# Performance work log

Measured on AMD Instinct MI355X. Metric: run time of the kernel, lower is better.

The kernel has to match this reference:

```python
import jax, jax.numpy as jnp
import numpy as np

B, IN, OUT = 8192, 1024, 1024
GRID_SIZE, SPLINE_ORDER = 5, 3
GRID_LO, GRID_HI = -1.0, 1.0
LN_EPS = 1e-5


def make_grid():
    h = (GRID_HI - GRID_LO) / GRID_SIZE
    g = jnp.linspace(GRID_LO - h * SPLINE_ORDER, GRID_HI + h * SPLINE_ORDER,
                     GRID_SIZE + 2 * SPLINE_ORDER + 1, dtype=jnp.float32)
    return jnp.broadcast_to(g, (IN, g.shape[0]))  # [IN, 12]


def setup_inputs() -> dict:
    key = jax.random.key(0)
    k1, k2, k3 = jax.random.split(key, 3)
    # kaiming_uniform_ linear: bound = sqrt(3/fan_in)
    bw_bound = float(np.sqrt(3.0 / IN))
    sw_bound = float(np.sqrt(3.0 / (IN * 8)))
    return {
        "x": jax.random.normal(k1, (B, IN), dtype=jnp.float32),
        "base_weight": jax.random.uniform(k2, (OUT, IN), minval=-bw_bound, maxval=bw_bound, dtype=jnp.float32),
        "spline_weight": jax.random.uniform(k3, (OUT, IN, GRID_SIZE + SPLINE_ORDER), minval=-sw_bound, maxval=sw_bound, dtype=jnp.float32),
        "grid": make_grid(),
        "ln_gamma": jnp.ones((OUT,), dtype=jnp.float32),
        "ln_beta": jnp.zeros((OUT,), dtype=jnp.float32),
        "prelu_a": jnp.full((1,), 0.25, dtype=jnp.float32),
    }


def _bspline_bases(x, grid):
    # x: [B, IN]; grid: [IN, 12] -> bases: [B, IN, GRID_SIZE+SPLINE_ORDER]
    xu = x[:, :, None]                      # [B, IN, 1]
    g = grid[None, :, :]                    # [1, IN, 12]
    bases = ((xu >= g[..., :-1]) & (xu < g[..., 1:])).astype(x.dtype)
    for k in range(1, SPLINE_ORDER + 1):
        left = g[..., :-(k + 1)]
        right = g[..., k:-1]
        g_rshift = g[..., k + 1:]
        g_lshift = g[..., 1:-k]
        dr = right - left
        dd = g_rshift - g_lshift
        dr = jnp.where(dr == 0, jnp.ones_like(dr), dr)
        dd = jnp.where(dd == 0, jnp.ones_like(dd), dd)
        bases = (xu - left) / dr * bases[..., :-1] + (g_rshift - xu) / dd * bases[..., 1:]
    return bases


def reference(x, base_weight, spline_weight, grid, ln_gamma, ln_beta, prelu_a):
    base_out = jnp.dot(jax.nn.gelu(x, approximate=False), base_weight.T)  # [B, OUT]
    bases = _bspline_bases(x, grid)                                        # [B, IN, 8]
    spline_out = jnp.einsum('bik,oik->bo', bases, spline_weight)           # [B, OUT]
    y = base_out + spline_out
    mu = jnp.mean(y, axis=-1, keepdims=True)
    var = jnp.mean(jnp.square(y - mu), axis=-1, keepdims=True)
    yn = (y - mu) * jax.lax.rsqrt(var + LN_EPS) * ln_gamma + ln_beta
    return jnp.where(yn >= 0, yn, prelu_a * yn)
```

## Files before the change

### kernel.cpp

```cpp
#include <hip/hip_runtime.h>
#include <hip/hip_bf16.h>

typedef __attribute__((ext_vector_type(8))) short bf16x8;
typedef __attribute__((ext_vector_type(4))) float f32x4;

#define KTOT 9216
#define KHALF 4608
#define NB   8192
#define NIN  1024
#define NOUT 1024

__device__ __forceinline__ void load_lds16(const void* g, void* l) {
  __builtin_amdgcn_global_load_lds(
      (const __attribute__((address_space(1))) void*)g,
      (__attribute__((address_space(3))) void*)l, 16, 0, 0);
}

__global__ void prep(const float* __restrict__ x,
                     const float* __restrict__ grid,
                     __hip_bfloat16* __restrict__ A,
                     const float* __restrict__ bw,
                     const float* __restrict__ sw,
                     __hip_bfloat16* __restrict__ W) {
  if (blockIdx.x < 4096) {
    const int tid = blockIdx.x * blockDim.x + threadIdx.x;
    const int i  = tid & (NIN - 1);
    const int b0 = (tid >> 10) << 3;

    float g[12];
#pragma unroll
    for (int j = 0; j < 12; ++j) g[j] = grid[j];

    float invdr1[10], invdd1[10], invdr2[9], invdd2[9], invdr3[8], invdd3[8];
#pragma unroll
    for (int j = 0; j < 10; ++j) {
      invdr1[j] = __builtin_amdgcn_rcpf(g[j + 1] - g[j]);
      invdd1[j] = __builtin_amdgcn_rcpf(g[j + 2] - g[j + 1]);
    }
#pragma unroll
    for (int j = 0; j < 9; ++j) {
      invdr2[j] = __builtin_amdgcn_rcpf(g[j + 2] - g[j]);
      invdd2[j] = __builtin_amdgcn_rcpf(g[j + 3] - g[j + 1]);
    }
#pragma unroll
    for (int j = 0; j < 8; ++j) {
      invdr3[j] = __builtin_amdgcn_rcpf(g[j + 3] - g[j]);
      invdd3[j] = __builtin_amdgcn_rcpf(g[j + 4] - g[j + 1]);
    }

    for (int bb = 0; bb < 8; ++bb) {
      const int b = b0 + bb;
      const float xv = x[(size_t)b * NIN + i];
      const float ge = 0.5f * xv * (1.0f + erff(xv * 0.70710678118654752f));
      __hip_bfloat16* Arow = A + (size_t)b * KTOT;
      Arow[i] = __float2bfloat16(ge);

      float bas[11];
#pragma unroll
      for (int j = 0; j < 11; ++j)
        bas[j] = (xv >= g[j] && xv < g[j + 1]) ? 1.0f : 0.0f;
#pragma unroll
      for (int j = 0; j < 10; ++j)
        bas[j] = (xv - g[j]) * invdr1[j] * bas[j] + (g[j + 2] - xv) * invdd1[j] * bas[j + 1];
#pragma unroll
      for (int j = 0; j < 9; ++j)
        bas[j] = (xv - g[j]) * invdr2[j] * bas[j] + (g[j + 3] - xv) * invdd2[j] * bas[j + 1];
#pragma unroll
      for (int j = 0; j < 8; ++j)
        bas[j] = (xv - g[j]) * invdr3[j] * bas[j] + (g[j + 4] - xv) * invdd3[j] * bas[j + 1];

      union { __hip_bfloat16 h[8]; uint4 v; } u;
#pragma unroll
      for (int k = 0; k < 8; ++k) u.h[k] = __float2bfloat16(bas[k]);
      *reinterpret_cast<uint4*>(Arow + NIN + i * 8) = u.v;
    }
  } else {
    const int idx = (blockIdx.x - 4096) * blockDim.x + threadIdx.x;
    const int o  = idx / 1152;
    const int c8 = (idx - o * 1152) * 8;
    const float* src = (c8 < 1024) ? (bw + (size_t)o * 1024 + c8)
                                   : (sw + (size_t)o * 8192 + (c8 - 1024));
    float4 f0 = reinterpret_cast<const float4*>(src)[0];
    float4 f1 = reinterpret_cast<const float4*>(src)[1];
    union { __hip_bfloat16 h[8]; uint4 v; } u;
    u.h[0] = __float2bfloat16(f0.x); u.h[1] = __float2bfloat16(f0.y);
    u.h[2] = __float2bfloat16(f0.z); u.h[3] = __float2bfloat16(f0.w);
    u.h[4] = __float2bfloat16(f1.x); u.h[5] = __float2bfloat16(f1.y);
    u.h[6] = __float2bfloat16(f1.z); u.h[7] = __float2bfloat16(f1.w);
    *reinterpret_cast<uint4*>(W + (size_t)o * KTOT + c8) = u.v;
  }
}

__global__ __launch_bounds__(512, 2)
void gemm_8ph(const __hip_bfloat16* __restrict__ A,
              const __hip_bfloat16* __restrict__ Bw,
              float* __restrict__ P0,
              float* __restrict__ P1w) {
  __shared__ char smem[131072];

  const int tid  = threadIdx.x;
  const int lane = tid & 63;
  const int wave = tid >> 6;
  const int wr = wave >> 2;
  const int wc = wave & 3;

  const int orig = blockIdx.x;
  const int bid  = (orig & 7) * 32 + (orig >> 3);
  const int ks    = bid & 1;
  const int tileN = (bid >> 1) & 3;
  const int tileM = bid >> 3;
  const size_t brow = (size_t)tileM * 256;
  const size_t bcol = (size_t)tileN * 256;
  const int kbeg = ks * KHALF;

  const __hip_bfloat16* Ab = A  + brow * KTOT;
  const __hip_bfloat16* Bb = Bw + bcol * KTOT;
  float* C = ks ? P1w : P0;

  const int swsrc = ((tid & 7) ^ ((tid >> 3) & 7)) * 8;
  const __hip_bfloat16* srcA = Ab + (size_t)(tid >> 3) * KTOT + kbeg + swsrc;
  const __hip_bfloat16* srcB = Bb + (size_t)(tid >> 3) * KTOT + kbeg + swsrc;
  const int wdst = wave * 1024;

  auto stageA = [&](int bf, int h, int kt) {
    const __hip_bfloat16* g = srcA + (size_t)h * (128 * KTOT) + (size_t)kt * 64;
    char* d = smem + (bf * 4 + h) * 16384 + wdst;
    load_lds16(g, d);
    load_lds16(g + (size_t)64 * KTOT, d + 8192);
  };
  auto stageB = [&](int bf, int h, int kt) {
    const __hip_bfloat16* g = srcB + (size_t)h * (128 * KTOT) + (size_t)kt * 64;
    char* d = smem + (bf * 4 + 2 + h) * 16384 + wdst;
    load_lds16(g, d);
    load_lds16(g + (size_t)64 * KTOT, d + 8192);
  };

  const int fr = lane & 15;
  const int hi = lane >> 4;
  const int sw = (fr & 7) << 4;
  const int ax0 = (hi * 16) ^ sw;
  const int ax1 = (64 + hi * 16) ^ sw;

  bf16x8 a[4][2], b[4][2];
  f32x4 acc[8][4] = {};

#define RD_A(CB, MH) { \
    const char* Ah = smem + ((CB) * 4 + wr) * 16384 + (MH) * 64 * 128; \
    _Pragma("unroll") \
    for (int mi2 = 0; mi2 < 4; ++mi2) { \
      const char* p = Ah + (mi2 * 16 + fr) * 128; \
      a[mi2][0] = *(const bf16x8*)(p + ax0); \
      a[mi2][1] = *(const bf16x8*)(p + ax1); } }

#define RD_B(CB, NH) { \
    const char* Bh = smem + ((CB) * 4 + 2 + (wc >> 1)) * 16384 + ((wc & 1) * 64 + (NH) * 32) * 128; \
    _Pragma("unroll") \
    for (int ni2 = 0; ni2 < 2; ++ni2) { \
      const char* p = Bh + (ni2 * 16 + fr) * 128; \
      b[(NH) * 2 + ni2][0] = *(const bf16x8*)(p + ax0); \
      b[(NH) * 2 + ni2][1] = *(const bf16x8*)(p + ax1); } }

#define SYNC1() do { \
    asm volatile("s_waitcnt lgkmcnt(0)" ::: "memory"); \
    __builtin_amdgcn_s_barrier(); \
    asm volatile("" ::: "memory"); } while (0)

#define QMFMA(MH, NH) do { \
    __builtin_amdgcn_s_setprio(1); \
    _Pragma("unroll") \
    for (int mi2 = 0; mi2 < 4; ++mi2) \
      _Pragma("unroll") \
      for (int ni2 = 0; ni2 < 2; ++ni2) \
        _Pragma("unroll") \
        for (int kk = 0; kk < 2; ++kk) \
          acc[(MH) * 4 + mi2][(NH) * 2 + ni2] = \
            __builtin_amdgcn_mfma_f32_16x16x32_bf16(a[mi2][kk], b[(NH) * 2 + ni2][kk], \
                                                    acc[(MH) * 4 + mi2][(NH) * 2 + ni2], 0, 0, 0); \
    __builtin_amdgcn_s_setprio(0); } while (0)

#define TILE(T, CB, STB, STA, VM1, VM2, VM4) do { \
     \
    RD_A(CB, 0); RD_B(CB, 0); \
    if (STB) stageB((CB) ^ 1, 0, (T) + 1); \
    asm volatile(VM1 ::: "memory"); \
    SYNC1(); QMFMA(0, 0); \
     \
    RD_B(CB, 1); \
    if (STB) stageB((CB) ^ 1, 1, (T) + 1); \
    asm volatile(VM2 ::: "memory"); \
    SYNC1(); QMFMA(0, 1); \
     \
    RD_A(CB, 1); \
    if (STA) stageA(CB, 0, (T) + 2); \
    SYNC1(); QMFMA(1, 1); \
     \
    if (STA) stageA(CB, 1, (T) + 2); \
    asm volatile(VM4 ::: "memory"); \
    SYNC1(); QMFMA(1, 0); \
  } while (0)

  stageA(0, 0, 0); stageA(0, 1, 0); stageB(0, 0, 0); stageB(0, 1, 0);
  stageA(1, 0, 1); stageA(1, 1, 1);
  asm volatile("s_waitcnt vmcnt(6)" ::: "memory");
  __builtin_amdgcn_s_barrier();
  asm volatile("" ::: "memory");

  for (int it = 0; it < 35; ++it) {
    const int t0 = it * 2;
    TILE(t0, 0, 1, 1,
         "s_waitcnt vmcnt(6)", "s_waitcnt vmcnt(6)", "s_waitcnt vmcnt(6)");
    TILE(t0 + 1, 1, 1, 1,
         "s_waitcnt vmcnt(6)", "s_waitcnt vmcnt(6)", "s_waitcnt vmcnt(6)");
  }
  TILE(70, 0, 1, 0,
       "s_waitcnt vmcnt(6)", "s_waitcnt vmcnt(6)", "s_waitcnt vmcnt(2)");
  TILE(71, 1, 0, 0,
       "s_waitcnt vmcnt(0)", "s_nop 0", "s_nop 0");

#undef TILE
#undef QMFMA
#undef SYNC1
#undef RD_B
#undef RD_A

  const int crow0 = (lane >> 4) * 4;
#pragma unroll
  for (int mi = 0; mi < 8; ++mi)
#pragma unroll
    for (int ni = 0; ni < 4; ++ni) {
      const size_t r0 = brow + wr * 128 + mi * 16 + crow0;
      const size_t cc = bcol + wc * 64 + ni * 16 + fr;
      float* cp = C + r0 * NOUT + cc;
#pragma unroll
      for (int r = 0; r < 4; ++r) cp[(size_t)r * NOUT] = acc[mi][ni][r];
    }
}

__global__ void reduce_ln_prelu(const float* __restrict__ P0,
                                float* __restrict__ y,
                                const float* __restrict__ gamma,
                                const float* __restrict__ beta,
                                const float* __restrict__ pa) {
  const int row = blockIdx.x;
  const int t = threadIdx.x;
  const float* p0r = P0 + (size_t)row * NOUT;
  float* yr = y + (size_t)row * NOUT;

  float4 aa = reinterpret_cast<const float4*>(p0r)[t];
  float4 v = reinterpret_cast<const float4*>(yr)[t];
  v.x += aa.x; v.y += aa.y; v.z += aa.z; v.w += aa.w;

  float s  = v.x + v.y + v.z + v.w;
  float sq = v.x * v.x + v.y * v.y + v.z * v.z + v.w * v.w;
#pragma unroll
  for (int off = 32; off > 0; off >>= 1) {
    s  += __shfl_down(s, off);
    sq += __shfl_down(sq, off);
  }
  __shared__ float red[8];
  const int wv = t >> 6, lane = t & 63;
  if (lane == 0) { red[wv] = s; red[4 + wv] = sq; }
  __syncthreads();
  if (t == 0) {
    const float S = red[0] + red[1] + red[2] + red[3];
    const float Q = red[4] + red[5] + red[6] + red[7];
    const float mu = S * (1.0f / NOUT);
    const float var = Q * (1.0f / NOUT) - mu * mu;
    red[0] = mu;
    red[1] = rsqrtf(var + 1e-5f);
  }
  __syncthreads();
  const float mu = red[0], rs = red[1];
  const float aP = pa[0];
  const float4 g4 = reinterpret_cast<const float4*>(gamma)[t];
  const float4 b4 = reinterpret_cast<const float4*>(beta)[t];
  float o0 = (v.x - mu) * rs * g4.x + b4.x;
  float o1 = (v.y - mu) * rs * g4.y + b4.y;
  float o2 = (v.z - mu) * rs * g4.z + b4.z;
  float o3 = (v.w - mu) * rs * g4.w + b4.w;
  v.x = o0 >= 0.0f ? o0 : aP * o0;
  v.y = o1 >= 0.0f ? o1 : aP * o1;
  v.z = o2 >= 0.0f ? o2 : aP * o2;
  v.w = o3 >= 0.0f ? o3 : aP * o3;
  reinterpret_cast<float4*>(yr)[t] = v;
}

extern "C" void kernel_launch(void* const* d_in, const int* in_sizes, int n_in,
                              void* d_out, int out_size, void* d_ws, size_t ws_size,
                              hipStream_t stream) {
  const float* x     = (const float*)d_in[0];
  const float* bw    = (const float*)d_in[1];
  const float* sw    = (const float*)d_in[2];
  const float* grid  = (const float*)d_in[3];
  const float* gamma = (const float*)d_in[4];
  const float* beta  = (const float*)d_in[5];
  const float* pa    = (const float*)d_in[6];
  float* out = (float*)d_out;

  __hip_bfloat16* Abuf = (__hip_bfloat16*)d_ws;
  __hip_bfloat16* Wbuf = Abuf + (size_t)NB * KTOT;
  float* P0 = (float*)(Wbuf + (size_t)NOUT * KTOT);

  prep<<<4096 + 4608, 256, 0, stream>>>(x, grid, Abuf, bw, sw, Wbuf);
  gemm_8ph<<<(NB / 256) * (NOUT / 256) * 2, 512, 0, stream>>>(Abuf, Wbuf, P0, out);
  reduce_ln_prelu<<<NB, 256, 0, stream>>>(P0, out, gamma, beta, pa);
}
```

Baseline: 202.4 us.

## Triple-buffer B tiles in dynamic LDS and reorder phase synchronization

Moves the GEMM's shared memory to a 160KB dynamic allocation, with a double-buffered A tile and a three-slot rotating B buffer. The main loop is unrolled by six to cycle the B slots, and staging now prefetches A one tile ahead and B two tiles ahead. The per-phase sync now places the barrier before the LDS-count wait and adds a scheduling barrier. This aims to hide global-load latency further, but the larger LDS footprint likely cuts residency to one block per CU.

```diff
diff --git a/kernel.cpp b/kernel.cpp
--- a/kernel.cpp
+++ b/kernel.cpp
@@ -96,7 +96,7 @@
               const __hip_bfloat16* __restrict__ Bw,
               float* __restrict__ P0,
               float* __restrict__ P1w) {
-  __shared__ char smem[131072];
+  extern __shared__ char smem[];
 
   const int tid  = threadIdx.x;
   const int lane = tid & 63;
@@ -122,15 +122,18 @@
   const __hip_bfloat16* srcB = Bb + (size_t)(tid >> 3) * KTOT + kbeg + swsrc;
   const int wdst = wave * 1024;
 
-  auto stageA = [&](int bf, int h, int kt) {
+#define AHALF(buf, h) (smem + (buf) * 32768 + (h) * 16384)
+#define BHALF(slot, h) (smem + 65536 + (slot) * 32768 + (h) * 16384)
+
+  auto stageA = [&](int bufA, int h, int kt) {
     const __hip_bfloat16* g = srcA + (size_t)h * (128 * KTOT) + (size_t)kt * 64;
-    char* d = smem + (bf * 4 + h) * 16384 + wdst;
+    char* d = AHALF(bufA, h) + wdst;
     load_lds16(g, d);
     load_lds16(g + (size_t)64 * KTOT, d + 8192);
   };
-  auto stageB = [&](int bf, int h, int kt) {
+  auto stageB = [&](int slot, int h, int kt) {
     const __hip_bfloat16* g = srcB + (size_t)h * (128 * KTOT) + (size_t)kt * 64;
-    char* d = smem + (bf * 4 + 2 + h) * 16384 + wdst;
+    char* d = BHALF(slot, h) + wdst;
     load_lds16(g, d);
     load_lds16(g + (size_t)64 * KTOT, d + 8192);
   };
@@ -144,26 +147,27 @@
   bf16x8 a[4][2], b[4][2];
   f32x4 acc[8][4] = {};
 
-#define RD_A(CB, MH) { \
-    const char* Ah = smem + ((CB) * 4 + wr) * 16384 + (MH) * 64 * 128; \
+#define RD_A(CBA, MH) { \
+    const char* Ah = AHALF(CBA, wr) + (MH) * 8192; \
     _Pragma("unroll") \
     for (int mi2 = 0; mi2 < 4; ++mi2) { \
       const char* p = Ah + (mi2 * 16 + fr) * 128; \
       a[mi2][0] = *(const bf16x8*)(p + ax0); \
       a[mi2][1] = *(const bf16x8*)(p + ax1); } }
 
-#define RD_B(CB, NH) { \
-    const char* Bh = smem + ((CB) * 4 + 2 + (wc >> 1)) * 16384 + ((wc & 1) * 64 + (NH) * 32) * 128; \
+#define RD_B(SB, NH) { \
+    const char* Bh = BHALF(SB, wc >> 1) + ((wc & 1) * 64 + (NH) * 32) * 128; \
     _Pragma("unroll") \
     for (int ni2 = 0; ni2 < 2; ++ni2) { \
       const char* p = Bh + (ni2 * 16 + fr) * 128; \
       b[(NH) * 2 + ni2][0] = *(const bf16x8*)(p + ax0); \
       b[(NH) * 2 + ni2][1] = *(const bf16x8*)(p + ax1); } }
 
-#define SYNC1() do { \
+#define PH_SYNC() do { \
+    asm volatile("" ::: "memory"); \
+    __builtin_amdgcn_s_barrier(); \
     asm volatile("s_waitcnt lgkmcnt(0)" ::: "memory"); \
-    __builtin_amdgcn_s_barrier(); \
-    asm volatile("" ::: "memory"); } while (0)
+    __builtin_amdgcn_sched_barrier(0); } while (0)
 
 #define QMFMA(MH, NH) do { \
     __builtin_amdgcn_s_setprio(1); \
@@ -178,50 +182,55 @@
                                                     acc[(MH) * 4 + mi2][(NH) * 2 + ni2], 0, 0, 0); \
     __builtin_amdgcn_s_setprio(0); } while (0)
 
-#define TILE(T, CB, STB, STA, VM1, VM2, VM4) do { \
+#define TILE(T, CBA, SB, SB2, STA, STB, VM2, VM4) do { \
      \
-    RD_A(CB, 0); RD_B(CB, 0); \
-    if (STB) stageB((CB) ^ 1, 0, (T) + 1); \
-    asm volatile(VM1 ::: "memory"); \
-    SYNC1(); QMFMA(0, 0); \
+    RD_A(CBA, 0); RD_B(SB, 0); \
+    if (STA) stageA((CBA) ^ 1, 0, (T) + 1); \
+    PH_SYNC(); QMFMA(0, 0); \
      \
-    RD_B(CB, 1); \
-    if (STB) stageB((CB) ^ 1, 1, (T) + 1); \
+    RD_B(SB, 1); \
+    if (STA) stageA((CBA) ^ 1, 1, (T) + 1); \
     asm volatile(VM2 ::: "memory"); \
-    SYNC1(); QMFMA(0, 1); \
+    PH_SYNC(); QMFMA(0, 1); \
      \
-    RD_A(CB, 1); \
-    if (STA) stageA(CB, 0, (T) + 2); \
-    SYNC1(); QMFMA(1, 1); \
+    RD_A(CBA, 1); \
+    if (STB) stageB(SB2, 0, (T) + 2); \
+    PH_SYNC(); QMFMA(1, 1); \
      \
-    if (STA) stageA(CB, 1, (T) + 2); \
+    if (STB) stageB(SB2, 1, (T) + 2); \
     asm volatile(VM4 ::: "memory"); \
-    SYNC1(); QMFMA(1, 0); \
+    PH_SYNC(); QMFMA(1, 0); \
   } while (0)
 
-  stageA(0, 0, 0); stageA(0, 1, 0); stageB(0, 0, 0); stageB(0, 1, 0);
-  stageA(1, 0, 1); stageA(1, 1, 1);
+  stageB(0, 0, 0); stageB(0, 1, 0);
+  stageA(0, 0, 0); stageA(0, 1, 0);
+  stageB(1, 0, 1); stageB(1, 1, 1);
   asm volatile("s_waitcnt vmcnt(6)" ::: "memory");
   __builtin_amdgcn_s_barrier();
   asm volatile("" ::: "memory");
 
-  for (int it = 0; it < 35; ++it) {
-    const int t0 = it * 2;
-    TILE(t0, 0, 1, 1,
-         "s_waitcnt vmcnt(6)", "s_waitcnt vmcnt(6)", "s_waitcnt vmcnt(6)");
-    TILE(t0 + 1, 1, 1, 1,
-         "s_waitcnt vmcnt(6)", "s_waitcnt vmcnt(6)", "s_waitcnt vmcnt(6)");
+  for (int it = 0; it < 11; ++it) {
+    TILE(it * 6 + 0, 0, 0, 2, 1, 1, "s_waitcnt vmcnt(8)", "s_waitcnt vmcnt(6)");
+    TILE(it * 6 + 1, 1, 1, 0, 1, 1, "s_waitcnt vmcnt(8)", "s_waitcnt vmcnt(6)");
+    TILE(it * 6 + 2, 0, 2, 1, 1, 1, "s_waitcnt vmcnt(8)", "s_waitcnt vmcnt(6)");
+    TILE(it * 6 + 3, 1, 0, 2, 1, 1, "s_waitcnt vmcnt(8)", "s_waitcnt vmcnt(6)");
+    TILE(it * 6 + 4, 0, 1, 0, 1, 1, "s_waitcnt vmcnt(8)", "s_waitcnt vmcnt(6)");
+    TILE(it * 6 + 5, 1, 2, 1, 1, 1, "s_waitcnt vmcnt(8)", "s_waitcnt vmcnt(6)");
   }
-  TILE(70, 0, 1, 0,
-       "s_waitcnt vmcnt(6)", "s_waitcnt vmcnt(6)", "s_waitcnt vmcnt(2)");
-  TILE(71, 1, 0, 0,
-       "s_waitcnt vmcnt(0)", "s_nop 0", "s_nop 0");
+  TILE(66, 0, 0, 2, 1, 1, "s_waitcnt vmcnt(8)", "s_waitcnt vmcnt(6)");
+  TILE(67, 1, 1, 0, 1, 1, "s_waitcnt vmcnt(8)", "s_waitcnt vmcnt(6)");
+  TILE(68, 0, 2, 1, 1, 1, "s_waitcnt vmcnt(8)", "s_waitcnt vmcnt(6)");
+  TILE(69, 1, 0, 2, 1, 1, "s_waitcnt vmcnt(8)", "s_waitcnt vmcnt(6)");
+  TILE(70, 0, 1, 0, 1, 0, "s_waitcnt vmcnt(8)", "s_waitcnt vmcnt(2)");
+  TILE(71, 1, 2, 1, 0, 0, "s_waitcnt vmcnt(0)", "s_nop 0");
 
 #undef TILE
 #undef QMFMA
-#undef SYNC1
+#undef PH_SYNC
 #undef RD_B
 #undef RD_A
+#undef BHALF
+#undef AHALF
 
   const int crow0 = (lane >> 4) * 4;
 #pragma unroll
@@ -301,7 +310,10 @@
   __hip_bfloat16* Wbuf = Abuf + (size_t)NB * KTOT;
   float* P0 = (float*)(Wbuf + (size_t)NOUT * KTOT);
 
+  hipFuncSetAttribute(reinterpret_cast<const void*>(gemm_8ph),
+                      hipFuncAttributeMaxDynamicSharedMemorySize, 163840);
+
   prep<<<4096 + 4608, 256, 0, stream>>>(x, grid, Abuf, bw, sw, Wbuf);
-  gemm_8ph<<<(NB / 256) * (NOUT / 256) * 2, 512, 0, stream>>>(Abuf, Wbuf, P0, out);
+  gemm_8ph<<<(NB / 256) * (NOUT / 256) * 2, 512, 163840, stream>>>(Abuf, Wbuf, P0, out);
   reduce_ln_prelu<<<NB, 256, 0, stream>>>(P0, out, gamma, beta, pa);
 }
```

Result: no change. 198.7 us (-1.9%).

## Load B fragments directly to registers and quad-buffer A in LDS

Applied to the files above, without the earlier changes.

The GEMM kernel stops staging the weight (B) tiles through shared memory. Each wave now loads its B fragments straight from global memory into registers, double-buffered across K tiles. A tiles use a 4-deep LDS ring covering the full 256-row tile, and each K step has one barrier instead of four. This cuts LDS traffic and synchronisation, but B fragments are re-read from global/L2 by every wave sharing a column and register pressure goes up, which may hurt occupancy.

```diff
diff --git a/kernel.cpp b/kernel.cpp
--- a/kernel.cpp
+++ b/kernel.cpp
@@ -92,10 +92,10 @@
 }
 
 __global__ __launch_bounds__(512, 2)
-void gemm_8ph(const __hip_bfloat16* __restrict__ A,
-              const __hip_bfloat16* __restrict__ Bw,
-              float* __restrict__ P0,
-              float* __restrict__ P1w) {
+void gemm_flat(const __hip_bfloat16* __restrict__ A,
+               const __hip_bfloat16* __restrict__ Bw,
+               float* __restrict__ P0,
+               float* __restrict__ P1w) {
   __shared__ char smem[131072];
 
   const int tid  = threadIdx.x;
@@ -114,25 +114,19 @@
   const int kbeg = ks * KHALF;
 
   const __hip_bfloat16* Ab = A  + brow * KTOT;
-  const __hip_bfloat16* Bb = Bw + bcol * KTOT;
   float* C = ks ? P1w : P0;
 
   const int swsrc = ((tid & 7) ^ ((tid >> 3) & 7)) * 8;
   const __hip_bfloat16* srcA = Ab + (size_t)(tid >> 3) * KTOT + kbeg + swsrc;
-  const __hip_bfloat16* srcB = Bb + (size_t)(tid >> 3) * KTOT + kbeg + swsrc;
   const int wdst = wave * 1024;
 
-  auto stageA = [&](int bf, int h, int kt) {
-    const __hip_bfloat16* g = srcA + (size_t)h * (128 * KTOT) + (size_t)kt * 64;
-    char* d = smem + (bf * 4 + h) * 16384 + wdst;
+  auto stageA = [&](int kt) {
+    const __hip_bfloat16* g = srcA + (size_t)kt * 64;
+    char* d = smem + ((kt & 3) * 32768) + wdst;
     load_lds16(g, d);
-    load_lds16(g + (size_t)64 * KTOT, d + 8192);
-  };
-  auto stageB = [&](int bf, int h, int kt) {
-    const __hip_bfloat16* g = srcB + (size_t)h * (128 * KTOT) + (size_t)kt * 64;
-    char* d = smem + (bf * 4 + 2 + h) * 16384 + wdst;
-    load_lds16(g, d);
-    load_lds16(g + (size_t)64 * KTOT, d + 8192);
+    load_lds16(g + (size_t)64  * KTOT, d + 8192);
+    load_lds16(g + (size_t)128 * KTOT, d + 16384);
+    load_lds16(g + (size_t)192 * KTOT, d + 24576);
   };
 
   const int fr = lane & 15;
@@ -141,87 +135,83 @@
   const int ax0 = (hi * 16) ^ sw;
   const int ax1 = (64 + hi * 16) ^ sw;
 
-  bf16x8 a[4][2], b[4][2];
+  const __hip_bfloat16* pB0 = Bw + (size_t)(bcol + wc * 64 + fr) * KTOT + kbeg + hi * 8;
+  const __hip_bfloat16* pB1 = pB0 + (size_t)16 * KTOT;
+  const __hip_bfloat16* pB2 = pB0 + (size_t)32 * KTOT;
+  const __hip_bfloat16* pB3 = pB0 + (size_t)48 * KTOT;
+
+  bf16x8 a[4][2], bE[4][2], bO[4][2];
   f32x4 acc[8][4] = {};
 
-#define RD_A(CB, MH) { \
-    const char* Ah = smem + ((CB) * 4 + wr) * 16384 + (MH) * 64 * 128; \
+#define LOADB(DST) do { \
+    DST[0][0] = *(const bf16x8*)(pB0); DST[0][1] = *(const bf16x8*)(pB0 + 32); \
+    DST[1][0] = *(const bf16x8*)(pB1); DST[1][1] = *(const bf16x8*)(pB1 + 32); \
+    DST[2][0] = *(const bf16x8*)(pB2); DST[2][1] = *(const bf16x8*)(pB2 + 32); \
+    DST[3][0] = *(const bf16x8*)(pB3); DST[3][1] = *(const bf16x8*)(pB3 + 32); \
+    pB0 += 64; pB1 += 64; pB2 += 64; pB3 += 64; } while (0)
+
+#define RD_A(BUF, MH) { \
+    const char* Ah = smem + (BUF) * 32768 + wr * 16384 + (MH) * 8192; \
     _Pragma("unroll") \
     for (int mi2 = 0; mi2 < 4; ++mi2) { \
       const char* p = Ah + (mi2 * 16 + fr) * 128; \
       a[mi2][0] = *(const bf16x8*)(p + ax0); \
       a[mi2][1] = *(const bf16x8*)(p + ax1); } }
 
-#define RD_B(CB, NH) { \
-    const char* Bh = smem + ((CB) * 4 + 2 + (wc >> 1)) * 16384 + ((wc & 1) * 64 + (NH) * 32) * 128; \
-    _Pragma("unroll") \
-    for (int ni2 = 0; ni2 < 2; ++ni2) { \
-      const char* p = Bh + (ni2 * 16 + fr) * 128; \
-      b[(NH) * 2 + ni2][0] = *(const bf16x8*)(p + ax0); \
-      b[(NH) * 2 + ni2][1] = *(const bf16x8*)(p + ax1); } }
-
-#define SYNC1() do { \
-    asm volatile("s_waitcnt lgkmcnt(0)" ::: "memory"); \
-    __builtin_amdgcn_s_barrier(); \
-    asm volatile("" ::: "memory"); } while (0)
-
-#define QMFMA(MH, NH) do { \
+#define MFMA_HALF(MH, CUR) do { \
     __builtin_amdgcn_s_setprio(1); \
     _Pragma("unroll") \
     for (int mi2 = 0; mi2 < 4; ++mi2) \
       _Pragma("unroll") \
-      for (int ni2 = 0; ni2 < 2; ++ni2) \
+      for (int ni2 = 0; ni2 < 4; ++ni2) \
         _Pragma("unroll") \
         for (int kk = 0; kk < 2; ++kk) \
-          acc[(MH) * 4 + mi2][(NH) * 2 + ni2] = \
-            __builtin_amdgcn_mfma_f32_16x16x32_bf16(a[mi2][kk], b[(NH) * 2 + ni2][kk], \
-                                                    acc[(MH) * 4 + mi2][(NH) * 2 + ni2], 0, 0, 0); \
+          acc[(MH) * 4 + mi2][ni2] = \
+            __builtin_amdgcn_mfma_f32_16x16x32_bf16(a[mi2][kk], CUR[ni2][kk], \
+                                                    acc[(MH) * 4 + mi2][ni2], 0, 0, 0); \
     __builtin_amdgcn_s_setprio(0); } while (0)
 
-#define TILE(T, CB, STB, STA, VM1, VM2, VM4) do { \
+#define TILE(BUF, CUR, NXT, DOB, STA, KT3, VM) do { \
      \
-    RD_A(CB, 0); RD_B(CB, 0); \
-    if (STB) stageB((CB) ^ 1, 0, (T) + 1); \
-    asm volatile(VM1 ::: "memory"); \
-    SYNC1(); QMFMA(0, 0); \
+    RD_A(BUF, 0); \
+    if (DOB) LOADB(NXT); \
+    asm volatile(VM ::: "memory"); \
+    __builtin_amdgcn_s_barrier(); \
+    asm volatile("s_waitcnt lgkmcnt(0)" ::: "memory"); \
+    __builtin_amdgcn_sched_barrier(0); \
+    MFMA_HALF(0, CUR); \
      \
-    RD_B(CB, 1); \
-    if (STB) stageB((CB) ^ 1, 1, (T) + 1); \
-    asm volatile(VM2 ::: "memory"); \
-    SYNC1(); QMFMA(0, 1); \
-     \
-    RD_A(CB, 1); \
-    if (STA) stageA(CB, 0, (T) + 2); \
-    SYNC1(); QMFMA(1, 1); \
-     \
-    if (STA) stageA(CB, 1, (T) + 2); \
-    asm volatile(VM4 ::: "memory"); \
-    SYNC1(); QMFMA(1, 0); \
+    RD_A(BUF, 1); \
+    if (STA) stageA(KT3); \
+    asm volatile("s_waitcnt lgkmcnt(0)" ::: "memory"); \
+    __builtin_amdgcn_sched_barrier(0); \
+    MFMA_HALF(1, CUR); \
   } while (0)
 
-  stageA(0, 0, 0); stageA(0, 1, 0); stageB(0, 0, 0); stageB(0, 1, 0);
-  stageA(1, 0, 1); stageA(1, 1, 1);
-  asm volatile("s_waitcnt vmcnt(6)" ::: "memory");
+  stageA(0);
+  stageA(1);
+  LOADB(bE);
+  stageA(2);
+  asm volatile("s_waitcnt vmcnt(12)" ::: "memory");
   __builtin_amdgcn_s_barrier();
   asm volatile("" ::: "memory");
 
-  for (int it = 0; it < 35; ++it) {
-    const int t0 = it * 2;
-    TILE(t0, 0, 1, 1,
-         "s_waitcnt vmcnt(6)", "s_waitcnt vmcnt(6)", "s_waitcnt vmcnt(6)");
-    TILE(t0 + 1, 1, 1, 1,
-         "s_waitcnt vmcnt(6)", "s_waitcnt vmcnt(6)", "s_waitcnt vmcnt(6)");
-  }
-  TILE(70, 0, 1, 0,
-       "s_waitcnt vmcnt(6)", "s_waitcnt vmcnt(6)", "s_waitcnt vmcnt(2)");
-  TILE(71, 1, 0, 0,
-       "s_waitcnt vmcnt(0)", "s_nop 0", "s_nop 0");
+  for (int it = 0; it < 17; ++it) {
+    const int t0 = it * 4;
+    TILE(0, bE, bO, 1, 1, t0 + 3, "s_waitcnt vmcnt(8)");
+    TILE(1, bO, bE, 1, 1, t0 + 4, "s_waitcnt vmcnt(8)");
+    TILE(2, bE, bO, 1, 1, t0 + 5, "s_waitcnt vmcnt(8)");
+    TILE(3, bO, bE, 1, 1, t0 + 6, "s_waitcnt vmcnt(8)");
+  }
+  TILE(0, bE, bO, 1, 1, 71, "s_waitcnt vmcnt(8)");
+  TILE(1, bO, bE, 1, 0, 0,  "s_waitcnt vmcnt(8)");
+  TILE(2, bE, bO, 1, 0, 0,  "s_waitcnt vmcnt(4)");
+  TILE(3, bO, bE, 0, 0, 0,  "s_waitcnt vmcnt(0)");
 
 #undef TILE
-#undef QMFMA
-#undef SYNC1
-#undef RD_B
+#undef MFMA_HALF
 #undef RD_A
+#undef LOADB
 
   const int crow0 = (lane >> 4) * 4;
 #pragma unroll
@@ -302,6 +292,6 @@
   float* P0 = (float*)(Wbuf + (size_t)NOUT * KTOT);
 
   prep<<<4096 + 4608, 256, 0, stream>>>(x, grid, Abuf, bw, sw, Wbuf);
-  gemm_8ph<<<(NB / 256) * (NOUT / 256) * 2, 512, 0, stream>>>(Abuf, Wbuf, P0, out);
+  gemm_flat<<<(NB / 256) * (NOUT / 256) * 2, 512, 0, stream>>>(Abuf, Wbuf, P0, out);
   reduce_ln_prelu<<<NB, 256, 0, stream>>>(P0, out, gamma, beta, pa);
 }
```

New measurement: 246.6 us. +21.8%, slower.
